# Optimization experiments

Measured on AMD Instinct MI355X. Metric: run time of the kernel, lower is better.

The kernel has to match this reference:

```python
import jax, jax.numpy as jnp
import numpy as np

BIN_NUM = 256
HIDDEN = 1024
B, S = 128, 1024
FEAT = BIN_NUM - 1          # 255
LAST = FEAT + 3             # 258, used as d_k in the original code


def setup_inputs() -> dict:
    key = jax.random.key(0)
    ks = jax.random.split(key, 8)

    def lin(k, out_d, in_d):
        # kaiming_uniform_ with relu nonlinearity: bound = sqrt(6/in_d)
        bound = np.sqrt(6.0 / in_d)
        return jax.random.uniform(k, (out_d, in_d), jnp.float32, -bound, bound)

    return {
        "input_tensor": jax.random.normal(ks[0], (B, S, LAST), jnp.float32),
        "kW": lin(ks[1], HIDDEN, FEAT), "kb": jnp.zeros((HIDDEN,), jnp.float32),
        "vW": lin(ks[2], HIDDEN, FEAT), "vb": jnp.zeros((HIDDEN,), jnp.float32),
        "qW": lin(ks[3], HIDDEN, 3),    "qb": jnp.zeros((HIDDEN,), jnp.float32),
        "W1": lin(ks[4], HIDDEN // 2, HIDDEN),      "b1": jnp.zeros((HIDDEN // 2,), jnp.float32),
        "W2": lin(ks[5], HIDDEN // 4, HIDDEN // 2), "b2": jnp.zeros((HIDDEN // 4,), jnp.float32),
        "W3": lin(ks[6], 2, HIDDEN // 4),           "b3": jnp.zeros((2,), jnp.float32),
    }


def reference(input_tensor, kW, kb, vW, vb, qW, qb, W1, b1, W2, b2, W3, b3):
    d_k = input_tensor.shape[-1]                      # NOTE: full last dim (258)
    feats = input_tensor[..., :FEAT]                  # [B,S,255]
    archi = input_tensor[:, 0, FEAT:][:, None, :]     # [B,1,3]

    k = jnp.einsum('bsf,hf->bsh', feats, kW) + kb     # [B,S,H]
    v = jnp.einsum('bsf,hf->bsh', feats, vW) + vb     # [B,S,H]
    q = jnp.einsum('bqf,hf->bqh', archi, qW) + qb     # [B,1,H]

    scores = jnp.einsum('bqh,bsh->bqs', q, k) / jnp.sqrt(jnp.float32(d_k))
    attn = jax.nn.softmax(scores, axis=-1)            # [B,1,S]
    res = jnp.einsum('bqs,bsh->bqh', attn, v)[:, 0, :]  # squeeze -> [B,H]

    # classifier (dropout is identity at inference)
    h = jax.nn.relu(res @ W1.T + b1)
    h = jax.nn.relu(h @ W2.T + b2)
    return h @ W3.T + b3                              # [B,2]
```

## Files before the change

### kernel.cpp

```cpp
#include <hip/hip_runtime.h>
#include <stdint.h>

#define NBATCH 128
#define SEQ    1024
#define ROWE   258
#define NPART  16

#define WS_KQP   0
#define WS_PART  524288
#define WS_WF    2654208
#define WS_REST  2785280
#define WS_H1P   3309568

static __device__ __forceinline__ float fexp2(float x){ return __builtin_amdgcn_exp2f(x); }

__global__ __launch_bounds__(256) void qk_kernel(const float* __restrict__ in,
    const float* __restrict__ kW, const float* __restrict__ qW,
    const float* __restrict__ qb, float* __restrict__ kqp,
    float* __restrict__ h1pre, float* __restrict__ out)
{
    __shared__ float qv[2][256];
    const int bb = blockIdx.x;
    const int hh = blockIdx.y;
    const int t  = threadIdx.x;
    const int b0 = bb * 2;
    if (hh == 0) {
        h1pre[(size_t)b0 * 512 + t]             = 0.f;
        h1pre[(size_t)b0 * 512 + 256 + t]       = 0.f;
        h1pre[(size_t)(b0 + 1) * 512 + t]       = 0.f;
        h1pre[(size_t)(b0 + 1) * 512 + 256 + t] = 0.f;
        if (t < 4) out[b0 * 2 + t] = 0.f;
    }
    const int h = hh * 256 + t;
    const float w0 = qW[h * 3 + 0], w1 = qW[h * 3 + 1], w2 = qW[h * 3 + 2], bq = qb[h];
    #pragma unroll
    for (int u = 0; u < 2; u++) {
        const size_t abase = (size_t)(b0 + u) * (SEQ * ROWE) + 255;
        qv[u][t] = bq + in[abase] * w0 + in[abase + 1] * w1 + in[abase + 2] * w2;
    }
    __syncthreads();
    const int col = (t < 255) ? t : 254;
    const float* kWp = kW + (size_t)(hh * 256) * 255 + col;
    float acc0 = 0.f, acc1 = 0.f;
    #pragma unroll 8
    for (int i = 0; i < 256; i++) {
        const float kv = kWp[(size_t)i * 255];
        acc0 = fmaf(qv[0][i], kv, acc0);
        acc1 = fmaf(qv[1][i], kv, acc1);
    }
    kqp[(size_t)((hh << 7) + b0) * 256 + t]       = (t < 255) ? acc0 : 0.f;
    kqp[(size_t)((hh << 7) + b0 + 1) * 256 + t]   = (t < 255) ? acc1 : 0.f;
}

__global__ __launch_bounds__(256) void attn_kernel(const float* __restrict__ in,
                                                   const float* __restrict__ kqp,
                                                   float* __restrict__ part)
{
    __shared__ float sm[4], sl[4], sacc[4][256];
    const int p = blockIdx.x, b = blockIdx.y;
    const int t = threadIdx.x, w = t >> 6, lane = t & 63;

    float2 k0 = make_float2(0.f, 0.f), k1 = make_float2(0.f, 0.f);
    #pragma unroll
    for (int hh = 0; hh < 4; hh++) {
        const float* pp = kqp + (size_t)((hh << 7) + b) * 256;
        const float2 u = *(const float2*)(pp + 2 * lane);
        const float2 v = *(const float2*)(pp + 128 + 2 * lane);
        k0.x += u.x; k0.y += u.y; k1.x += v.x; k1.y += v.y;
    }
    const float SCALE = (float)(1.4426950408889634 / 16.062378404209142);
    k0.x *= SCALE; k0.y *= SCALE; k1.x *= SCALE; k1.y *= SCALE;

    const float* rp = in + ((size_t)b * SEQ + p * 64 + w) * ROWE;
    float m = -INFINITY, l = 0.f;
    float a0 = 0.f, a1 = 0.f, a2 = 0.f, a3 = 0.f;

    float2 x = *(const float2*)(rp + 2 * lane);
    float2 y = *(const float2*)(rp + 128 + 2 * lane);
    #pragma unroll
    for (int i = 0; i < 16; i++) {
        const float e0 = x.x, e1 = x.y, e2 = y.x, e3 = y.y;
        if (i < 15) {
            rp += 4 * ROWE;
            x = *(const float2*)(rp + 2 * lane);
            y = *(const float2*)(rp + 128 + 2 * lane);
        }
        float d = fmaf(e0, k0.x, fmaf(e1, k0.y, fmaf(e2, k1.x, e3 * k1.y)));
        #pragma unroll
        for (int off = 32; off > 0; off >>= 1) d += __shfl_xor(d, off, 64);
        const float mn = fmaxf(m, d);
        const float cc = fexp2(m - mn);
        const float wt = fexp2(d - mn);
        l  = fmaf(l, cc, wt);
        a0 = fmaf(a0, cc, wt * e0);
        a1 = fmaf(a1, cc, wt * e1);
        a2 = fmaf(a2, cc, wt * e2);
        a3 = fmaf(a3, cc, wt * e3);
        m = mn;
    }

    ((float2*)(sacc[w]))[lane]       = make_float2(a0, a1);
    ((float2*)(sacc[w] + 128))[lane] = make_float2(a2, a3);
    if (lane == 0) { sm[w] = m; sl[w] = l; }
    __syncthreads();

    const float M  = fmaxf(fmaxf(sm[0], sm[1]), fmaxf(sm[2], sm[3]));
    const float c0 = fexp2(sm[0] - M), c1 = fexp2(sm[1] - M);
    const float c2 = fexp2(sm[2] - M), c3 = fexp2(sm[3] - M);
    const float acc = c0 * sacc[0][t] + c1 * sacc[1][t] + c2 * sacc[2][t] + c3 * sacc[3][t];
    float* o = part + ((size_t)b * NPART + p) * 260;
    o[t] = acc;
    if (t == 0) {
        o[256] = M;
        o[257] = c0 * sl[0] + c1 * sl[1] + c2 * sl[2] + c3 * sl[3];
    }
}

__global__ __launch_bounds__(256) void comb_kernel(const float* __restrict__ part,
                                                   float* __restrict__ wf)
{
    const int b = blockIdx.x, t = threadIdx.x;
    const float* pb = part + (size_t)b * NPART * 260;
    float M = -INFINITY;
    #pragma unroll
    for (int p = 0; p < NPART; p++) M = fmaxf(M, pb[p * 260 + 256]);
    float L = 0.f, acc = 0.f;
    #pragma unroll
    for (int p = 0; p < NPART; p++) {
        const float cc = fexp2(pb[p * 260 + 256] - M);
        L   = fmaf(cc, pb[p * 260 + 257], L);
        acc = fmaf(cc, pb[p * 260 + t], acc);
    }
    wf[b * 256 + t] = (t < 255) ? acc / L : 0.f;
}

__global__ __launch_bounds__(512) void res_kernel(const float* __restrict__ vW,
                                                  const float* __restrict__ vb,
                                                  const float* __restrict__ wf,
                                                  float* __restrict__ resT)
{
    __shared__ float vws[8][256];
    __shared__ float wfs[64][130];
    const int g = blockIdx.x, t = threadIdx.x;
    #pragma unroll
    for (int i = 0; i < 4; i++) {
        const int idx = i * 512 + t, f = idx & 255, hh = idx >> 8;
        vws[hh][f] = (f < 255) ? vW[(g * 8 + hh) * 255 + f] : 0.f;
    }
    const int b = t & 127, ho = t >> 7;
    const int fl = t & 63, wv = t >> 6;
    float acc0 = 0.f, acc1 = 0.f;
    for (int c = 0; c < 4; c++) {
        __syncthreads();
        #pragma unroll
        for (int i = 0; i < 16; i++) {
            const int bb = i * 8 + wv;
            wfs[fl][bb] = wf[bb * 256 + c * 64 + fl];
        }
        __syncthreads();
        #pragma unroll 8
        for (int f = 0; f < 64; f++) {
            const float w2 = wfs[f][b];
            acc0 = fmaf(w2, vws[ho][c * 64 + f], acc0);
            acc1 = fmaf(w2, vws[ho + 4][c * 64 + f], acc1);
        }
    }
    const int h0 = g * 8 + ho, h1 = h0 + 4;
    resT[h0 * 128 + b] = acc0 + vb[h0];
    resT[h1 * 128 + b] = acc1 + vb[h1];
}

__global__ __launch_bounds__(256) void h1_kernel(const float* __restrict__ W1,
                                                 const float* __restrict__ resT,
                                                 float* __restrict__ h1pre)
{
    __shared__ float W1s[16][256];
    __shared__ float ress[64][66];
    const int j0 = blockIdx.x * 16, b0 = blockIdx.y * 64, h0 = blockIdx.z * 256;
    const int t = threadIdx.x;
    #pragma unroll
    for (int i = 0; i < 16; i++) {
        const int idx = i * 256 + t, hl = idx & 255, jj = idx >> 8;
        W1s[jj][hl] = W1[(j0 + jj) * 1024 + h0 + hl];
    }
    const int bb = t & 63, jg = t >> 6;
    float acc[4] = {0.f, 0.f, 0.f, 0.f};
    for (int sc = 0; sc < 4; sc++) {
        __syncthreads();
        {
            const int bl = t & 63, wvv = t >> 6;
            #pragma unroll
            for (int i = 0; i < 16; i++) {
                const int hl = i * 4 + wvv;
                ress[hl][bl] = resT[(h0 + sc * 64 + hl) * 128 + b0 + bl];
            }
        }
        __syncthreads();
        #pragma unroll 4
        for (int hl = 0; hl < 64; hl++) {
            const float rv = ress[hl][bb];
            acc[0] = fmaf(rv, W1s[jg * 4 + 0][sc * 64 + hl], acc[0]);
            acc[1] = fmaf(rv, W1s[jg * 4 + 1][sc * 64 + hl], acc[1]);
            acc[2] = fmaf(rv, W1s[jg * 4 + 2][sc * 64 + hl], acc[2]);
            acc[3] = fmaf(rv, W1s[jg * 4 + 3][sc * 64 + hl], acc[3]);
        }
    }
    #pragma unroll
    for (int k = 0; k < 4; k++)
        atomicAdd(&h1pre[(size_t)(b0 + bb) * 512 + j0 + jg * 4 + k], acc[k]);
}

__global__ __launch_bounds__(256) void h2out_kernel(const float* __restrict__ W2,
    const float* __restrict__ b1, const float* __restrict__ b2,
    const float* __restrict__ W3, const float* __restrict__ b3,
    const float* __restrict__ h1pre, float* __restrict__ out)
{
    __shared__ float W2s[8][512];
    __shared__ float h1s[64][66];
    __shared__ float po[4][64][2];
    const int j20 = blockIdx.x * 8, b0 = blockIdx.y * 64;
    const int t = threadIdx.x;
    #pragma unroll
    for (int i = 0; i < 16; i++) {
        const int idx = i * 256 + t, jl = idx & 511, jj = idx >> 9;
        W2s[jj][jl] = W2[(j20 + jj) * 512 + jl];
    }
    const int bb = t & 63, jg = t >> 6;
    float acc[2] = {0.f, 0.f};
    for (int sc = 0; sc < 8; sc++) {
        __syncthreads();
        {
            const int jl = t & 63, wvv = t >> 6;
            #pragma unroll
            for (int i = 0; i < 16; i++) {
                const int bl = i * 4 + wvv;
                const float v = h1pre[(size_t)(b0 + bl) * 512 + sc * 64 + jl] + b1[sc * 64 + jl];
                h1s[jl][bl] = fmaxf(v, 0.f);
            }
        }
        __syncthreads();
        #pragma unroll 4
        for (int jl = 0; jl < 64; jl++) {
            const float hv = h1s[jl][bb];
            acc[0] = fmaf(hv, W2s[jg * 2 + 0][sc * 64 + jl], acc[0]);
            acc[1] = fmaf(hv, W2s[jg * 2 + 1][sc * 64 + jl], acc[1]);
        }
    }
    float p0 = 0.f, p1 = 0.f;
    #pragma unroll
    for (int k = 0; k < 2; k++) {
        const int j2 = j20 + jg * 2 + k;
        const float h2v = fmaxf(acc[k] + b2[j2], 0.f);
        p0 = fmaf(h2v, W3[j2],       p0);
        p1 = fmaf(h2v, W3[256 + j2], p1);
    }
    po[jg][bb][0] = p0;
    po[jg][bb][1] = p1;
    __syncthreads();
    if (t < 128) {
        const int b = t & 63, o = t >> 6;
        float s = po[0][b][o] + po[1][b][o] + po[2][b][o] + po[3][b][o];
        if (blockIdx.x == 0) s += b3[o];
        atomicAdd(&out[(b0 + b) * 2 + o], s);
    }
}

extern "C" void kernel_launch(void* const* d_in, const int* in_sizes, int n_in,
                              void* d_out, int out_size, void* d_ws, size_t ws_size,
                              hipStream_t stream)
{
    (void)in_sizes; (void)n_in; (void)out_size; (void)ws_size;
    const float* in = (const float*)d_in[0];
    const float* kW = (const float*)d_in[1];
    const float* vW = (const float*)d_in[3];
    const float* vb = (const float*)d_in[4];
    const float* qW = (const float*)d_in[5];
    const float* qb = (const float*)d_in[6];
    const float* W1 = (const float*)d_in[7];
    const float* b1 = (const float*)d_in[8];
    const float* W2 = (const float*)d_in[9];
    const float* b2 = (const float*)d_in[10];
    const float* W3 = (const float*)d_in[11];
    const float* b3 = (const float*)d_in[12];

    char* ws = (char*)d_ws;
    float* kqp   = (float*)(ws + WS_KQP);
    float* part  = (float*)(ws + WS_PART);
    float* wf    = (float*)(ws + WS_WF);
    float* resT  = (float*)(ws + WS_REST);
    float* h1pre = (float*)(ws + WS_H1P);

    qk_kernel   <<<dim3(64, 4),        256, 0, stream>>>(in, kW, qW, qb, kqp, h1pre, (float*)d_out);
    attn_kernel <<<dim3(NPART, NBATCH), 256, 0, stream>>>(in, kqp, part);
    comb_kernel <<<128,                256, 0, stream>>>(part, wf);
    res_kernel  <<<128,                512, 0, stream>>>(vW, vb, wf, resT);
    h1_kernel   <<<dim3(32, 2, 4),     256, 0, stream>>>(W1, resT, h1pre);
    h2out_kernel<<<dim3(32, 2),        256, 0, stream>>>(W2, b1, b2, W3, b3, h1pre, (float*)d_out);
}
```

Baseline: 288.8 us.

## Remap attention so each half-wave processes one row with 8 elements per lane

The attention kernel now assigns 32 lanes per sequence row with 8 contiguous elements each, so each wave handles two rows at once and the dot-product reduction needs five shuffle steps instead of six. The per-block merge now combines eight partial softmax states instead of four. Each lane issues more independent loads per step, aiming for better memory-level parallelism on the streaming input. It also raises the qk loop unroll and adds an occupancy hint, at the cost of more registers per thread.

```diff
diff --git a/kernel.cpp b/kernel.cpp
--- a/kernel.cpp
+++ b/kernel.cpp
@@ -11,6 +11,7 @@
 #define WS_WF    2654208
 #define WS_REST  2785280
 #define WS_H1P   3309568
+
 
 static __device__ __forceinline__ float fexp2(float x){ return __builtin_amdgcn_exp2f(x); }
 
@@ -42,7 +43,7 @@
     const int col = (t < 255) ? t : 254;
     const float* kWp = kW + (size_t)(hh * 256) * 255 + col;
     float acc0 = 0.f, acc1 = 0.f;
-    #pragma unroll 8
+    #pragma unroll 16
     for (int i = 0; i < 256; i++) {
         const float kv = kWp[(size_t)i * 255];
         acc0 = fmaf(qv[0][i], kv, acc0);
@@ -52,68 +53,92 @@
     kqp[(size_t)((hh << 7) + b0 + 1) * 256 + t]   = (t < 255) ? acc1 : 0.f;
 }
 
-__global__ __launch_bounds__(256) void attn_kernel(const float* __restrict__ in,
-                                                   const float* __restrict__ kqp,
-                                                   float* __restrict__ part)
-{
-    __shared__ float sm[4], sl[4], sacc[4][256];
+__global__ __launch_bounds__(256, 8) void attn_kernel(const float* __restrict__ in,
+                                                      const float* __restrict__ kqp,
+                                                      float* __restrict__ part)
+{
+    __shared__ float sM[8], sL[8], sacc[8][256];
     const int p = blockIdx.x, b = blockIdx.y;
     const int t = threadIdx.x, w = t >> 6, lane = t & 63;
-
-    float2 k0 = make_float2(0.f, 0.f), k1 = make_float2(0.f, 0.f);
-    #pragma unroll
-    for (int hh = 0; hh < 4; hh++) {
-        const float* pp = kqp + (size_t)((hh << 7) + b) * 256;
-        const float2 u = *(const float2*)(pp + 2 * lane);
-        const float2 v = *(const float2*)(pp + 128 + 2 * lane);
-        k0.x += u.x; k0.y += u.y; k1.x += v.x; k1.y += v.y;
-    }
+    const int hf = lane >> 5, sub = lane & 31;
+
     const float SCALE = (float)(1.4426950408889634 / 16.062378404209142);
-    k0.x *= SCALE; k0.y *= SCALE; k1.x *= SCALE; k1.y *= SCALE;
-
-    const float* rp = in + ((size_t)b * SEQ + p * 64 + w) * ROWE;
+    float k[8];
+    {
+        float s0x=0.f,s0y=0.f,s0z=0.f,s0w=0.f, s1x=0.f,s1y=0.f,s1z=0.f,s1w=0.f;
+        #pragma unroll
+        for (int hh = 0; hh < 4; hh++) {
+            const float4* pp = (const float4*)(kqp + (size_t)((hh << 7) + b) * 256 + sub * 8);
+            const float4 u = pp[0], v = pp[1];
+            s0x+=u.x; s0y+=u.y; s0z+=u.z; s0w+=u.w;
+            s1x+=v.x; s1y+=v.y; s1z+=v.z; s1w+=v.w;
+        }
+        k[0]=s0x*SCALE; k[1]=s0y*SCALE; k[2]=s0z*SCALE; k[3]=s0w*SCALE;
+        k[4]=s1x*SCALE; k[5]=s1y*SCALE; k[6]=s1z*SCALE; k[7]=s1w*SCALE;
+    }
+
+    const float* rp = in + ((size_t)b * SEQ + p * 64 + w * 16 + hf) * ROWE + sub * 8;
+
+    float x[8], xn[8], a[8];
+    #pragma unroll
+    for (int j = 0; j < 8; j++) a[j] = 0.f;
+    #pragma unroll
+    for (int j = 0; j < 8; j += 2) {
+        const float2 v2 = *(const float2*)(rp + j);
+        x[j] = v2.x; x[j+1] = v2.y;
+    }
+    rp += 2 * ROWE;
     float m = -INFINITY, l = 0.f;
-    float a0 = 0.f, a1 = 0.f, a2 = 0.f, a3 = 0.f;
-
-    float2 x = *(const float2*)(rp + 2 * lane);
-    float2 y = *(const float2*)(rp + 128 + 2 * lane);
-    #pragma unroll
-    for (int i = 0; i < 16; i++) {
-        const float e0 = x.x, e1 = x.y, e2 = y.x, e3 = y.y;
-        if (i < 15) {
-            rp += 4 * ROWE;
-            x = *(const float2*)(rp + 2 * lane);
-            y = *(const float2*)(rp + 128 + 2 * lane);
-        }
-        float d = fmaf(e0, k0.x, fmaf(e1, k0.y, fmaf(e2, k1.x, e3 * k1.y)));
+
+    #pragma unroll
+    for (int i = 0; i < 8; i++) {
+        if (i < 7) {
+            #pragma unroll
+            for (int j = 0; j < 8; j += 2) {
+                const float2 v2 = *(const float2*)(rp + j);
+                xn[j] = v2.x; xn[j+1] = v2.y;
+            }
+            rp += 2 * ROWE;
+        }
+        const float d0 = fmaf(x[0], k[0], x[1] * k[1]);
+        const float d1 = fmaf(x[2], k[2], x[3] * k[3]);
+        const float d2 = fmaf(x[4], k[4], x[5] * k[5]);
+        const float d3 = fmaf(x[6], k[6], x[7] * k[7]);
+        float d = (d0 + d1) + (d2 + d3);
         #pragma unroll
-        for (int off = 32; off > 0; off >>= 1) d += __shfl_xor(d, off, 64);
+        for (int off = 16; off > 0; off >>= 1) d += __shfl_xor(d, off, 64);
         const float mn = fmaxf(m, d);
         const float cc = fexp2(m - mn);
         const float wt = fexp2(d - mn);
-        l  = fmaf(l, cc, wt);
-        a0 = fmaf(a0, cc, wt * e0);
-        a1 = fmaf(a1, cc, wt * e1);
-        a2 = fmaf(a2, cc, wt * e2);
-        a3 = fmaf(a3, cc, wt * e3);
+        l = fmaf(l, cc, wt);
+        #pragma unroll
+        for (int j = 0; j < 8; j++) a[j] = fmaf(a[j], cc, wt * x[j]);
         m = mn;
-    }
-
-    ((float2*)(sacc[w]))[lane]       = make_float2(a0, a1);
-    ((float2*)(sacc[w] + 128))[lane] = make_float2(a2, a3);
-    if (lane == 0) { sm[w] = m; sl[w] = l; }
+        if (i < 7) {
+            #pragma unroll
+            for (int j = 0; j < 8; j++) x[j] = xn[j];
+        }
+    }
+
+    const int id = w * 2 + hf;
+    #pragma unroll
+    for (int j = 0; j < 8; j += 2)
+        *(float2*)(&sacc[id][sub * 8 + j]) = make_float2(a[j], a[j+1]);
+    if (sub == 0) { sM[id] = m; sL[id] = l; }
     __syncthreads();
 
-    const float M  = fmaxf(fmaxf(sm[0], sm[1]), fmaxf(sm[2], sm[3]));
-    const float c0 = fexp2(sm[0] - M), c1 = fexp2(sm[1] - M);
-    const float c2 = fexp2(sm[2] - M), c3 = fexp2(sm[3] - M);
-    const float acc = c0 * sacc[0][t] + c1 * sacc[1][t] + c2 * sacc[2][t] + c3 * sacc[3][t];
+    float M = sM[0];
+    #pragma unroll
+    for (int q = 1; q < 8; q++) M = fmaxf(M, sM[q]);
+    float c[8];
+    #pragma unroll
+    for (int q = 0; q < 8; q++) c[q] = fexp2(sM[q] - M);
+    float acc = 0.f, Lm = 0.f;
+    #pragma unroll
+    for (int q = 0; q < 8; q++) { acc = fmaf(c[q], sacc[q][t], acc); Lm = fmaf(c[q], sL[q], Lm); }
     float* o = part + ((size_t)b * NPART + p) * 260;
     o[t] = acc;
-    if (t == 0) {
-        o[256] = M;
-        o[257] = c0 * sl[0] + c1 * sl[1] + c2 * sl[2] + c3 * sl[3];
-    }
+    if (t == 0) { o[256] = M; o[257] = Lm; }
 }
 
 __global__ __launch_bounds__(256) void comb_kernel(const float* __restrict__ part,
@@ -290,10 +315,10 @@
     float* resT  = (float*)(ws + WS_REST);
     float* h1pre = (float*)(ws + WS_H1P);
 
-    qk_kernel   <<<dim3(64, 4),        256, 0, stream>>>(in, kW, qW, qb, kqp, h1pre, (float*)d_out);
+    qk_kernel   <<<dim3(64, 4),         256, 0, stream>>>(in, kW, qW, qb, kqp, h1pre, (float*)d_out);
     attn_kernel <<<dim3(NPART, NBATCH), 256, 0, stream>>>(in, kqp, part);
-    comb_kernel <<<128,                256, 0, stream>>>(part, wf);
-    res_kernel  <<<128,                512, 0, stream>>>(vW, vb, wf, resT);
-    h1_kernel   <<<dim3(32, 2, 4),     256, 0, stream>>>(W1, resT, h1pre);
-    h2out_kernel<<<dim3(32, 2),        256, 0, stream>>>(W2, b1, b2, W3, b3, h1pre, (float*)d_out);
-}
+    comb_kernel <<<128,                 256, 0, stream>>>(part, wf);
+    res_kernel  <<<128,                 512, 0, stream>>>(vW, vb, wf, resT);
+    h1_kernel   <<<dim3(32, 2, 4),      256, 0, stream>>>(W1, resT, h1pre);
+    h2out_kernel<<<dim3(32, 2),         256, 0, stream>>>(W2, b1, b2, W3, b3, h1pre, (float*)d_out);
+}
```

New measurement: 322.1 us. 1.12x slower.
